# Performance work log

Measured on AMD Instinct MI355X. Metric: run time of the kernel, lower is better.

## Reference

```python
import jax, jax.numpy as jnp
import numpy as np

B, S, E, H, R = 2, 2048, 1024, 16, 8
D = E // H  # head depth = 64


def setup_inputs() -> dict:
    key = jax.random.key(0)
    ks = jax.random.split(key, 16)
    sd = 1.0 / np.sqrt(E)
    inp = {
        'q': jax.random.normal(ks[0], (B, S, E), jnp.float32),
        'k': jax.random.normal(ks[1], (B, S, E), jnp.float32),
        'v': jax.random.normal(ks[2], (B, S, E), jnp.float32),
        # Q projection (Dense + LoRA)
        'wq': jax.random.normal(ks[3], (E, E), jnp.float32) * sd,
        'bq': jnp.zeros((E,), jnp.float32),
        'wq_a': jax.random.normal(ks[4], (E, R), jnp.float32) * sd,
        'wq_b': jax.random.normal(ks[5], (R, E), jnp.float32) * 0.01,
        # K projection (plain Dense)
        'wk': jax.random.normal(ks[6], (E, E), jnp.float32) * sd,
        'bk': jnp.zeros((E,), jnp.float32),
        # V projection (Dense + LoRA)
        'wv': jax.random.normal(ks[7], (E, E), jnp.float32) * sd,
        'bv': jnp.zeros((E,), jnp.float32),
        'wv_a': jax.random.normal(ks[8], (E, R), jnp.float32) * sd,
        'wv_b': jax.random.normal(ks[9], (R, E), jnp.float32) * 0.01,
        # output projection
        'wo': jax.random.normal(ks[10], (E, E), jnp.float32) * sd,
        'bo': jnp.zeros((E,), jnp.float32),
    }
    return inp


def _lora_dense(x, w, b, w_a, w_b):
    # Dense(x) + (x @ A) @ B
    return x @ w + b + (x @ w_a) @ w_b


def _split_heads(x):
    # [B,S,E] -> [B,H,S,D]
    return x.reshape(B, S, H, D).transpose(0, 2, 1, 3)


def reference(q, k, v, wq, bq, wq_a, wq_b, wk, bk, wv, bv, wv_a, wv_b, wo, bo):
    qh = _split_heads(_lora_dense(q, wq, bq, wq_a, wq_b))
    kh = _split_heads(k @ wk + bk)
    vh = _split_heads(_lora_dense(v, wv, bv, wv_a, wv_b))
    # scaled dot-product attention per head
    scale = 1.0 / jnp.sqrt(jnp.asarray(D, jnp.float32))
    logits = jnp.einsum('bhqd,bhkd->bhqk', qh, kh) * scale
    attn = jax.nn.softmax(logits, axis=-1)
    out = jnp.einsum('bhqk,bhkd->bhqd', attn, vh)  # [B,H,S,D]
    out = out.transpose(0, 2, 1, 3).reshape(B, S, E)
    return out @ wo + bo
```

## Files before the change

kernel.cpp:

```cpp
#include <hip/hip_runtime.h>

typedef __attribute__((ext_vector_type(8))) _Float16 f16x8;
typedef __attribute__((ext_vector_type(4))) _Float16 f16x4;
typedef __attribute__((ext_vector_type(4))) float f32x4;

static __device__ __forceinline__ f16x4 pack4(float a, float b, float c, float d) {
    f16x4 r;
    auto p0 = __builtin_amdgcn_cvt_pkrtz(a, b);
    auto p1 = __builtin_amdgcn_cvt_pkrtz(c, d);
    r[0] = p0[0]; r[1] = p0[1]; r[2] = p1[0]; r[3] = p1[1];
    return r;
}

static __device__ __forceinline__ f16x8 cvt8(float4 u0, float4 u1) {
    f16x8 r;
    auto p = __builtin_amdgcn_cvt_pkrtz(u0.x, u0.y); r[0] = p[0]; r[1] = p[1];
    p = __builtin_amdgcn_cvt_pkrtz(u0.z, u0.w);      r[2] = p[0]; r[3] = p[1];
    p = __builtin_amdgcn_cvt_pkrtz(u1.x, u1.y);      r[4] = p[0]; r[5] = p[1];
    p = __builtin_amdgcn_cvt_pkrtz(u1.z, u1.w);      r[6] = p[0]; r[7] = p[1];
    return r;
}

static __device__ __forceinline__ void gll16(const void* g, void* l) {
    __builtin_amdgcn_global_load_lds(
        (const __attribute__((address_space(1))) unsigned int*)g,
        (__attribute__((address_space(3))) unsigned int*)l, 16, 0, 0);
}

__global__ __launch_bounds__(256) void prep16(const float* __restrict__ q, const float* __restrict__ k,
                                              const float* __restrict__ v, _Float16* __restrict__ o) {
    const float* X = blockIdx.y == 0 ? q : blockIdx.y == 1 ? k : v;
    _Float16* O = o + (size_t)blockIdx.y * 4194304;
    const int i = (blockIdx.x * 256 + threadIdx.x) * 8;
    *(f16x8*)&O[i] = cvt8(*(const float4*)&X[i], *(const float4*)&X[i + 4]);
}

__global__ __launch_bounds__(256) void tsplit_w16(const float* __restrict__ w0, const float* __restrict__ w1,
                                                  const float* __restrict__ w2, const float* __restrict__ w3,
                                                  _Float16* __restrict__ th) {
    const float* W = blockIdx.z == 0 ? w0 : blockIdx.z == 1 ? w1 : blockIdx.z == 2 ? w2 : w3;
    _Float16* oh = th + (size_t)blockIdx.z * 1048576;
    __shared__ float t[64][65];
    const int tid = threadIdx.x;
    const int kt = blockIdx.x, nb = blockIdx.y;
    const int k0 = kt * 64, n0 = nb * 64;
    const int c = tid & 15, r = tid >> 4;
#pragma unroll
    for (int i = 0; i < 4; ++i) {
        const int row = r + i * 16;
        const float4 v4 = *(const float4*)&W[(size_t)(k0 + row) * 1024 + n0 + c * 4];
        t[c * 4 + 0][row] = v4.x;
        t[c * 4 + 1][row] = v4.y;
        t[c * 4 + 2][row] = v4.z;
        t[c * 4 + 3][row] = v4.w;
    }
    __syncthreads();
    const size_t tb = (size_t)(nb * 16 + kt) * 4096;
#pragma unroll
    for (int i = 0; i < 2; ++i) {
        const int cid = tid * 2 + i;
        const int rr = cid >> 3, cc = cid & 7;
        const int ksrc = (cc ^ (rr & 7)) * 8;
        f16x8 hv;
#pragma unroll
        for (int j = 0; j < 8; ++j) hv[j] = (_Float16)t[rr][ksrc + j];
        *(f16x8*)&oh[tb + cid * 8] = hv;
    }
}

__global__ __launch_bounds__(256) void lora_xa2(const float* __restrict__ X0, const float* __restrict__ WA0,
                                                float* __restrict__ XA0,
                                                const float* __restrict__ X1, const float* __restrict__ WA1,
                                                float* __restrict__ XA1) {
    const float* X = blockIdx.y == 0 ? X0 : X1;
    const float* WA = blockIdx.y == 0 ? WA0 : WA1;
    float* XA = blockIdx.y == 0 ? XA0 : XA1;
    const int tid = threadIdx.x;
    const int w = tid >> 6, lane = tid & 63;
    const int m = blockIdx.x * 4 + w;
    const float* xrow = X + (size_t)m * 1024;
    float s[8] = {};
#pragma unroll
    for (int i = 0; i < 4; ++i) {
        const int k = lane * 4 + i * 256;
        const float4 x4 = *(const float4*)&xrow[k];
        const float xs[4] = {x4.x, x4.y, x4.z, x4.w};
#pragma unroll
        for (int j = 0; j < 4; ++j) {
            const float* wr = WA + (size_t)(k + j) * 8;
            const float xv = xs[j];
#pragma unroll
            for (int rr = 0; rr < 8; ++rr) s[rr] = fmaf(xv, wr[rr], s[rr]);
        }
    }
#pragma unroll
    for (int rr = 0; rr < 8; ++rr) {
        float v = s[rr];
        v += __shfl_xor(v, 32);
        v += __shfl_xor(v, 16);
        v += __shfl_xor(v, 8);
        v += __shfl_xor(v, 4);
        v += __shfl_xor(v, 2);
        v += __shfl_xor(v, 1);
        if (lane == 0) XA[(size_t)m * 8 + rr] = v;
    }
}

template <int OUT, bool LORA>
__global__ __launch_bounds__(256) void gemm_v3(const _Float16* __restrict__ A,
                                               const _Float16* __restrict__ Bt,
                                               const float* __restrict__ bias,
                                               const float* __restrict__ XA,
                                               const float* __restrict__ WB,
                                               float scale,
                                               void* __restrict__ outp) {
    __shared__ _Float16 Ahs[2][4096], Bhs[2][4096];
    const int tid = threadIdx.x;
    const int w = tid >> 6, l = tid & 63;
    const int lm = l & 15, g = l >> 4;
    const int wm = w >> 1, wn = w & 1;
    const int m0 = blockIdx.x * 64, nb = blockIdx.y, n0 = nb * 64;

    const int lr = l >> 3;
    const int ksw = ((l & 7) ^ lr) * 8;
    const _Float16* Asrc0 = A + (size_t)(m0 + w * 16 + lr) * 1024 + ksw;
    const _Float16* Asrc1 = A + (size_t)(m0 + w * 16 + 8 + lr) * 1024 + ksw;
    const _Float16* Bsrc0 = Bt + (size_t)nb * 65536 + (w * 128 + l) * 8;
    const _Float16* Bsrc1 = Bt + (size_t)nb * 65536 + (w * 128 + 64 + l) * 8;
    const int adst0 = w * 1024, adst1 = w * 1024 + 512;

    int afo[2][2], bfo[2][2];
#pragma unroll
    for (int t = 0; t < 2; ++t)
#pragma unroll
        for (int kc = 0; kc < 2; ++kc) {
            const int ar = wm * 32 + t * 16 + lm;
            const int br = wn * 32 + t * 16 + lm;
            afo[t][kc] = ar * 64 + (((kc * 4 + g) ^ (ar & 7)) * 8);
            bfo[t][kc] = br * 64 + (((kc * 4 + g) ^ (br & 7)) * 8);
        }

    f32x4 acc[2][2] = {};

#define STAGE(buf, kt)                                  \
    {                                                   \
        const int ko = (kt) * 64;                       \
        const int bo = (kt) * 4096;                     \
        gll16(Asrc0 + ko, &Ahs[buf][adst0]);            \
        gll16(Asrc1 + ko, &Ahs[buf][adst1]);            \
        gll16(Bsrc0 + bo, &Bhs[buf][adst0]);            \
        gll16(Bsrc1 + bo, &Bhs[buf][adst1]);            \
    }

    STAGE(0, 0)
    __syncthreads();

    for (int kt = 0; kt < 16; ++kt) {
        const int cur = kt & 1;
        if (kt < 15) STAGE(cur ^ 1, kt + 1)
        const _Float16* Ac = &Ahs[cur][0];
        const _Float16* Bc = &Bhs[cur][0];
#pragma unroll
        for (int kc = 0; kc < 2; ++kc) {
            f16x8 ah[2], bh[2];
#pragma unroll
            for (int i = 0; i < 2; ++i) {
                ah[i] = *(const f16x8*)&Ac[afo[i][kc]];
                bh[i] = *(const f16x8*)&Bc[bfo[i][kc]];
            }
            __builtin_amdgcn_s_setprio(1);
#pragma unroll
            for (int mt = 0; mt < 2; ++mt)
#pragma unroll
                for (int nt = 0; nt < 2; ++nt)
                    acc[mt][nt] = __builtin_amdgcn_mfma_f32_16x16x32_f16(ah[mt], bh[nt], acc[mt][nt], 0, 0, 0);
            __builtin_amdgcn_s_setprio(0);
        }
        __syncthreads();
    }
#undef STAGE

    const int nbase = n0 + wn * 32;
    const int head = nb;
    float bias2[2];
#pragma unroll
    for (int nt = 0; nt < 2; ++nt) bias2[nt] = bias[nbase + nt * 16 + lm];
    float wbv[8][2];
    if (LORA) {
#pragma unroll
        for (int rr = 0; rr < 8; ++rr)
#pragma unroll
            for (int nt = 0; nt < 2; ++nt) wbv[rr][nt] = WB[rr * 1024 + nbase + nt * 16 + lm];
    }
#pragma unroll
    for (int mt = 0; mt < 2; ++mt) {
        float ov[2][4];
#pragma unroll
        for (int r = 0; r < 4; ++r) {
            const int m = m0 + wm * 32 + mt * 16 + g * 4 + r;
            float xa8[8];
            if (LORA) {
#pragma unroll
                for (int rr = 0; rr < 8; ++rr) xa8[rr] = XA[(size_t)m * 8 + rr];
            }
#pragma unroll
            for (int nt = 0; nt < 2; ++nt) {
                float o = acc[mt][nt][r] + bias2[nt];
                if (LORA) {
#pragma unroll
                    for (int rr = 0; rr < 8; ++rr) o = fmaf(xa8[rr], wbv[rr][nt], o);
                }
                o *= scale;
                ov[nt][r] = o;
                if (OUT == 0) {
                    ((float*)outp)[(size_t)m * 1024 + nbase + nt * 16 + lm] = o;
                } else if (OUT == 1) {
                    const int b = m >> 11, s = m & 2047;
                    ((_Float16*)outp)[((size_t)(b * 16 + head) * 2048 + s) * 64 + wn * 32 + nt * 16 + lm] = (_Float16)o;
                }
            }
        }
        if (OUT == 2) {
            const int b = m0 >> 11;
            const int sb = (m0 & 2047) + wm * 32 + mt * 16 + g * 4;
#pragma unroll
            for (int nt = 0; nt < 2; ++nt) {
                const int d = wn * 32 + nt * 16 + lm;
                const f16x4 pv = pack4(ov[nt][0], ov[nt][1], ov[nt][2], ov[nt][3]);
                *(f16x4*)&((_Float16*)outp)[((size_t)(b * 16 + head) * 64 + d) * 2048 + sb] = pv;
            }
        }
    }
}

__global__ __launch_bounds__(256, 2) void flash_attn9(const _Float16* __restrict__ qh,
                                                      const _Float16* __restrict__ kh,
                                                      const _Float16* __restrict__ vT,
                                                      _Float16* __restrict__ ao) {
    __shared__ _Float16 Ks[2][4096];
    __shared__ _Float16 Vs[2][4096];
    const int tid = threadIdx.x;
    const int w = tid >> 6, l = tid & 63;
    const int m = l & 15, g = l >> 4;
    const int bh = blockIdx.x & 31, qt = blockIdx.x >> 5;
    const _Float16* Qb = qh + (size_t)bh * 131072;
    const _Float16* Kb = kh + (size_t)bh * 131072;
    const _Float16* Vb = vT + (size_t)bh * 131072;
    const int q0 = qt * 128 + w * 32;

    f16x8 qf[2][2];
#pragma unroll
    for (int qg = 0; qg < 2; ++qg) {
        const _Float16* qrow = Qb + (size_t)(q0 + qg * 16 + m) * 64 + g * 8;
        qf[qg][0] = *(const f16x8*)(qrow);
        qf[qg][1] = *(const f16x8*)(qrow + 32);
    }

    const int r0 = tid >> 3, c0 = tid & 7;
    const int r1 = (tid + 256) >> 3;
    const int kgl0 = r0 * 64 + c0 * 8;
    const int kgl1 = r1 * 64 + c0 * 8;
    const int kso0 = r0 * 64 + ((c0 ^ (r0 & 7)) * 8);
    const int kso1 = r1 * 64 + ((c0 ^ (r1 & 7)) * 8);
    const size_t vgl0 = (size_t)r0 * 2048 + c0 * 8;
    const size_t vgl1 = (size_t)r1 * 2048 + c0 * 8;

    int koff[4][2];
#pragma unroll
    for (int nt = 0; nt < 4; ++nt)
#pragma unroll
        for (int kc = 0; kc < 2; ++kc) {
            const int kv = nt * 16 + m;
            koff[nt][kc] = kv * 64 + (((kc * 4 + g) ^ (kv & 7)) * 8);
        }
    int voff[4][4];
#pragma unroll
    for (int dt = 0; dt < 4; ++dt)
#pragma unroll
        for (int nt = 0; nt < 4; ++nt) {
            const int d = dt * 16 + m;
            voff[dt][nt] = d * 64 + (((nt * 2 + (g >> 1)) ^ (d & 7)) * 8) + (g & 1) * 4;
        }

    f32x4 acc_o[2][4] = {};
    f32x4 acc_l[2] = {};
    const f16x4 onesf = {(_Float16)1.f, (_Float16)1.f, (_Float16)1.f, (_Float16)1.f};

    {
        const f16x8 ka = *(const f16x8*)(Kb + kgl0);
        const f16x8 kb2 = *(const f16x8*)(Kb + kgl1);
        const f16x8 va = *(const f16x8*)(Vb + vgl0);
        const f16x8 vb2 = *(const f16x8*)(Vb + vgl1);
        *(f16x8*)(&Ks[0][0] + kso0) = ka;
        *(f16x8*)(&Ks[0][0] + kso1) = kb2;
        *(f16x8*)(&Vs[0][0] + kso0) = va;
        *(f16x8*)(&Vs[0][0] + kso1) = vb2;
    }
    __syncthreads();

    for (int t = 0; t < 32; ++t) {
        const int cur = t & 1;
        f16x8 ka, kb2, va, vb2;
        if (t < 31) {
            const int koI = (t + 1) * 4096;
            const int voI = (t + 1) * 64;
            ka = *(const f16x8*)(Kb + koI + kgl0);
            kb2 = *(const f16x8*)(Kb + koI + kgl1);
            va = *(const f16x8*)(Vb + voI + vgl0);
            vb2 = *(const f16x8*)(Vb + voI + vgl1);
        }

        const _Float16* Kc = &Ks[cur][0];
        const _Float16* Vc = &Vs[cur][0];

        f32x4 s[2][4] = {};
        __builtin_amdgcn_s_setprio(1);
#pragma unroll
        for (int nt = 0; nt < 4; ++nt)
#pragma unroll
            for (int kc = 0; kc < 2; ++kc) {
                const f16x8 kf = *(const f16x8*)(Kc + koff[nt][kc]);
                s[0][nt] = __builtin_amdgcn_mfma_f32_16x16x32_f16(kf, qf[0][kc], s[0][nt], 0, 0, 0);
                s[1][nt] = __builtin_amdgcn_mfma_f32_16x16x32_f16(kf, qf[1][kc], s[1][nt], 0, 0, 0);
            }
        __builtin_amdgcn_s_setprio(0);

        f16x4 pf[2][4];
#pragma unroll
        for (int qg = 0; qg < 2; ++qg)
#pragma unroll
            for (int nt = 0; nt < 4; ++nt)
                pf[qg][nt] = pack4(exp2f(s[qg][nt][0]), exp2f(s[qg][nt][1]),
                                   exp2f(s[qg][nt][2]), exp2f(s[qg][nt][3]));

        __builtin_amdgcn_s_setprio(1);
#pragma unroll
        for (int nt = 0; nt < 4; ++nt) {
            acc_l[0] = __builtin_amdgcn_mfma_f32_16x16x16f16(onesf, pf[0][nt], acc_l[0], 0, 0, 0);
            acc_l[1] = __builtin_amdgcn_mfma_f32_16x16x16f16(onesf, pf[1][nt], acc_l[1], 0, 0, 0);
#pragma unroll
            for (int dt = 0; dt < 4; ++dt) {
                const f16x4 vf = *(const f16x4*)(Vc + voff[dt][nt]);
                acc_o[0][dt] = __builtin_amdgcn_mfma_f32_16x16x16f16(vf, pf[0][nt], acc_o[0][dt], 0, 0, 0);
                acc_o[1][dt] = __builtin_amdgcn_mfma_f32_16x16x16f16(vf, pf[1][nt], acc_o[1][dt], 0, 0, 0);
            }
        }
        __builtin_amdgcn_s_setprio(0);

        if (t < 31) {
            const int nxt = cur ^ 1;
            *(f16x8*)(&Ks[nxt][0] + kso0) = ka;
            *(f16x8*)(&Ks[nxt][0] + kso1) = kb2;
            *(f16x8*)(&Vs[nxt][0] + kso0) = va;
            *(f16x8*)(&Vs[nxt][0] + kso1) = vb2;
        }
        __syncthreads();
    }

    const int b = bh >> 4, h = bh & 15;
#pragma unroll
    for (int qg = 0; qg < 2; ++qg) {
        const float inv = 1.f / acc_l[qg][0];
        const int srow = q0 + qg * 16 + m;
        _Float16* orow = ao + ((size_t)(b * 2048 + srow)) * 1024 + h * 64;
#pragma unroll
        for (int dt = 0; dt < 4; ++dt) {
            const f16x4 o = pack4(acc_o[qg][dt][0] * inv, acc_o[qg][dt][1] * inv,
                                  acc_o[qg][dt][2] * inv, acc_o[qg][dt][3] * inv);
            *(f16x4*)&orow[dt * 16 + g * 4] = o;
        }
    }
}

extern "C" void kernel_launch(void* const* d_in, const int* in_sizes, int n_in,
                              void* d_out, int out_size, void* d_ws, size_t ws_size,
                              hipStream_t stream) {
    const float* q    = (const float*)d_in[0];
    const float* k    = (const float*)d_in[1];
    const float* v    = (const float*)d_in[2];
    const float* wq   = (const float*)d_in[3];
    const float* bq   = (const float*)d_in[4];
    const float* wq_a = (const float*)d_in[5];
    const float* wq_b = (const float*)d_in[6];
    const float* wk   = (const float*)d_in[7];
    const float* bk   = (const float*)d_in[8];
    const float* wv   = (const float*)d_in[9];
    const float* bv   = (const float*)d_in[10];
    const float* wv_a = (const float*)d_in[11];
    const float* wv_b = (const float*)d_in[12];
    const float* wo   = (const float*)d_in[13];
    const float* bo   = (const float*)d_in[14];
    float* out = (float*)d_out;

    char* wsb = (char*)d_ws;
    _Float16* Wt   = (_Float16*)(wsb);
    _Float16* a16  = (_Float16*)(wsb + (8u << 20));
    _Float16* aoF  = a16;
    _Float16* qhF  = (_Float16*)(wsb + (32u << 20));
    _Float16* khF  = (_Float16*)(wsb + (40u << 20));
    _Float16* vTF  = (_Float16*)(wsb + (48u << 20));
    float* xaq     = (float*)(wsb + (56u << 20));
    float* xav     = (float*)(wsb + (56u << 20) + (128u << 10));

    const dim3 ggrid(64, 16);
    const float qscale = 0.18033688f;

    tsplit_w16<<<dim3(16, 16, 4), 256, 0, stream>>>(wq, wk, wv, wo, Wt);
    lora_xa2<<<dim3(1024, 2), 256, 0, stream>>>(q, wq_a, xaq, v, wv_a, xav);
    prep16<<<dim3(2048, 3), 256, 0, stream>>>(q, k, v, a16);

    gemm_v3<1, true><<<ggrid, 256, 0, stream>>>(a16, Wt, bq, xaq, wq_b, qscale, qhF);
    gemm_v3<1, false><<<ggrid, 256, 0, stream>>>(a16 + 4194304, Wt + 1048576, bk, nullptr, nullptr, 1.f, khF);
    gemm_v3<2, true><<<ggrid, 256, 0, stream>>>(a16 + 8388608, Wt + 2097152, bv, xav, wv_b, 1.f, vTF);

    flash_attn9<<<512, 256, 0, stream>>>(qhF, khF, vTF, aoF);

    gemm_v3<0, false><<<ggrid, 256, 0, stream>>>(aoF, Wt + 3145728, bo, nullptr, nullptr, 1.f, out);
}
```

Measured before the change: 170.4 us.

## Use 128x64 GEMM tiles with 32x32x16 MFMA instructions

The projection GEMMs now compute a 128x64 output tile per block instead of 64x64, halving the grid and reusing each staged B tile across twice as many rows. The inner loop switches from 16x16x32 MFMAs to 32x32x16 MFMAs, each wave producing a 64x32 sub-tile, and the epilogue index mapping is rewritten for the new accumulator layout. This cuts B-operand global and LDS traffic per output and issues fewer, larger MFMAs. In exchange it uses more LDS and registers per block and launches 512 blocks instead of 1024, which may lower occupancy and load balance across CUs.

```diff
diff --git a/kernel.cpp b/kernel.cpp
--- a/kernel.cpp
+++ b/kernel.cpp
@@ -3,6 +3,7 @@
 typedef __attribute__((ext_vector_type(8))) _Float16 f16x8;
 typedef __attribute__((ext_vector_type(4))) _Float16 f16x4;
 typedef __attribute__((ext_vector_type(4))) float f32x4;
+typedef __attribute__((ext_vector_type(16))) float f32x16;
 
 static __device__ __forceinline__ f16x4 pack4(float a, float b, float c, float d) {
     f16x4 r;
@@ -107,49 +108,57 @@
 }
 
 template <int OUT, bool LORA>
-__global__ __launch_bounds__(256) void gemm_v3(const _Float16* __restrict__ A,
+__global__ __launch_bounds__(256) void gemm_v5(const _Float16* __restrict__ A,
                                                const _Float16* __restrict__ Bt,
                                                const float* __restrict__ bias,
                                                const float* __restrict__ XA,
                                                const float* __restrict__ WB,
                                                float scale,
                                                void* __restrict__ outp) {
-    __shared__ _Float16 Ahs[2][4096], Bhs[2][4096];
+    __shared__ _Float16 Ahs[2][8192];
+    __shared__ _Float16 Bhs[2][4096];
     const int tid = threadIdx.x;
     const int w = tid >> 6, l = tid & 63;
-    const int lm = l & 15, g = l >> 4;
+    const int ln = l & 31, hi = l >> 5;
     const int wm = w >> 1, wn = w & 1;
-    const int m0 = blockIdx.x * 64, nb = blockIdx.y, n0 = nb * 64;
+    const int m0 = blockIdx.x * 128, nb = blockIdx.y;
 
     const int lr = l >> 3;
     const int ksw = ((l & 7) ^ lr) * 8;
-    const _Float16* Asrc0 = A + (size_t)(m0 + w * 16 + lr) * 1024 + ksw;
-    const _Float16* Asrc1 = A + (size_t)(m0 + w * 16 + 8 + lr) * 1024 + ksw;
+    const _Float16* Asrc[4];
+    int adst[4];
+#pragma unroll
+    for (int j = 0; j < 4; ++j) {
+        Asrc[j] = A + (size_t)(m0 + w * 32 + j * 8 + lr) * 1024 + ksw;
+        adst[j] = w * 2048 + j * 512;
+    }
     const _Float16* Bsrc0 = Bt + (size_t)nb * 65536 + (w * 128 + l) * 8;
     const _Float16* Bsrc1 = Bt + (size_t)nb * 65536 + (w * 128 + 64 + l) * 8;
-    const int adst0 = w * 1024, adst1 = w * 1024 + 512;
-
-    int afo[2][2], bfo[2][2];
-#pragma unroll
-    for (int t = 0; t < 2; ++t)
-#pragma unroll
-        for (int kc = 0; kc < 2; ++kc) {
-            const int ar = wm * 32 + t * 16 + lm;
-            const int br = wn * 32 + t * 16 + lm;
-            afo[t][kc] = ar * 64 + (((kc * 4 + g) ^ (ar & 7)) * 8);
-            bfo[t][kc] = br * 64 + (((kc * 4 + g) ^ (br & 7)) * 8);
-        }
-
-    f32x4 acc[2][2] = {};
-
-#define STAGE(buf, kt)                                  \
-    {                                                   \
-        const int ko = (kt) * 64;                       \
-        const int bo = (kt) * 4096;                     \
-        gll16(Asrc0 + ko, &Ahs[buf][adst0]);            \
-        gll16(Asrc1 + ko, &Ahs[buf][adst1]);            \
-        gll16(Bsrc0 + bo, &Bhs[buf][adst0]);            \
-        gll16(Bsrc1 + bo, &Bhs[buf][adst1]);            \
+    const int bdst0 = w * 1024, bdst1 = w * 1024 + 512;
+
+    int afo[2][4], bfo[4];
+#pragma unroll
+    for (int s = 0; s < 4; ++s) {
+        const int c = s * 2 + hi;
+#pragma unroll
+        for (int mt = 0; mt < 2; ++mt) {
+            const int ar = wm * 64 + mt * 32 + ln;
+            afo[mt][s] = ar * 64 + ((c ^ (ln & 7)) * 8);
+        }
+        const int br = wn * 32 + ln;
+        bfo[s] = br * 64 + ((c ^ (ln & 7)) * 8);
+    }
+
+    f32x16 acc[2] = {};
+
+#define STAGE(buf, kt)                                       \
+    {                                                        \
+        const int ko = (kt) * 64;                            \
+        const int bo = (kt) * 4096;                          \
+        _Pragma("unroll") for (int j = 0; j < 4; ++j)        \
+            gll16(Asrc[j] + ko, &Ahs[buf][adst[j]]);         \
+        gll16(Bsrc0 + bo, &Bhs[buf][bdst0]);                 \
+        gll16(Bsrc1 + bo, &Bhs[buf][bdst1]);                 \
     }
 
     STAGE(0, 0)
@@ -161,73 +170,64 @@
         const _Float16* Ac = &Ahs[cur][0];
         const _Float16* Bc = &Bhs[cur][0];
 #pragma unroll
-        for (int kc = 0; kc < 2; ++kc) {
-            f16x8 ah[2], bh[2];
-#pragma unroll
-            for (int i = 0; i < 2; ++i) {
-                ah[i] = *(const f16x8*)&Ac[afo[i][kc]];
-                bh[i] = *(const f16x8*)&Bc[bfo[i][kc]];
-            }
+        for (int s = 0; s < 4; ++s) {
+            const f16x8 a0 = *(const f16x8*)&Ac[afo[0][s]];
+            const f16x8 a1 = *(const f16x8*)&Ac[afo[1][s]];
+            const f16x8 bfrag = *(const f16x8*)&Bc[bfo[s]];
             __builtin_amdgcn_s_setprio(1);
-#pragma unroll
-            for (int mt = 0; mt < 2; ++mt)
-#pragma unroll
-                for (int nt = 0; nt < 2; ++nt)
-                    acc[mt][nt] = __builtin_amdgcn_mfma_f32_16x16x32_f16(ah[mt], bh[nt], acc[mt][nt], 0, 0, 0);
+            acc[0] = __builtin_amdgcn_mfma_f32_32x32x16_f16(a0, bfrag, acc[0], 0, 0, 0);
+            acc[1] = __builtin_amdgcn_mfma_f32_32x32x16_f16(a1, bfrag, acc[1], 0, 0, 0);
             __builtin_amdgcn_s_setprio(0);
         }
         __syncthreads();
     }
 #undef STAGE
 
-    const int nbase = n0 + wn * 32;
-    const int head = nb;
-    float bias2[2];
-#pragma unroll
-    for (int nt = 0; nt < 2; ++nt) bias2[nt] = bias[nbase + nt * 16 + lm];
-    float wbv[8][2];
+    const int nl = nb * 64 + wn * 32 + ln;
+    const float biasl = bias[nl];
+    float wbl[8];
     if (LORA) {
 #pragma unroll
-        for (int rr = 0; rr < 8; ++rr)
-#pragma unroll
-            for (int nt = 0; nt < 2; ++nt) wbv[rr][nt] = WB[rr * 1024 + nbase + nt * 16 + lm];
+        for (int rr = 0; rr < 8; ++rr) wbl[rr] = WB[rr * 1024 + nl];
     }
 #pragma unroll
     for (int mt = 0; mt < 2; ++mt) {
-        float ov[2][4];
-#pragma unroll
-        for (int r = 0; r < 4; ++r) {
-            const int m = m0 + wm * 32 + mt * 16 + g * 4 + r;
-            float xa8[8];
-            if (LORA) {
-#pragma unroll
-                for (int rr = 0; rr < 8; ++rr) xa8[rr] = XA[(size_t)m * 8 + rr];
-            }
-#pragma unroll
-            for (int nt = 0; nt < 2; ++nt) {
-                float o = acc[mt][nt][r] + bias2[nt];
+        const int bm = m0 + wm * 64 + mt * 32;
+#pragma unroll
+        for (int q2 = 0; q2 < 4; ++q2) {
+            float ov[4];
+#pragma unroll
+            for (int r4 = 0; r4 < 4; ++r4) {
+                const int reg = q2 * 4 + r4;
+                const int m = bm + r4 + 8 * q2 + 4 * hi;
+                float o = acc[mt][reg] + biasl;
                 if (LORA) {
-#pragma unroll
-                    for (int rr = 0; rr < 8; ++rr) o = fmaf(xa8[rr], wbv[rr][nt], o);
+                    const float4 xa0 = *(const float4*)&XA[(size_t)m * 8];
+                    const float4 xa1 = *(const float4*)&XA[(size_t)m * 8 + 4];
+                    o = fmaf(xa0.x, wbl[0], o);
+                    o = fmaf(xa0.y, wbl[1], o);
+                    o = fmaf(xa0.z, wbl[2], o);
+                    o = fmaf(xa0.w, wbl[3], o);
+                    o = fmaf(xa1.x, wbl[4], o);
+                    o = fmaf(xa1.y, wbl[5], o);
+                    o = fmaf(xa1.z, wbl[6], o);
+                    o = fmaf(xa1.w, wbl[7], o);
                 }
                 o *= scale;
-                ov[nt][r] = o;
+                ov[r4] = o;
                 if (OUT == 0) {
-                    ((float*)outp)[(size_t)m * 1024 + nbase + nt * 16 + lm] = o;
+                    ((float*)outp)[(size_t)m * 1024 + nl] = o;
                 } else if (OUT == 1) {
                     const int b = m >> 11, s = m & 2047;
-                    ((_Float16*)outp)[((size_t)(b * 16 + head) * 2048 + s) * 64 + wn * 32 + nt * 16 + lm] = (_Float16)o;
+                    ((_Float16*)outp)[((size_t)(b * 16 + nb) * 2048 + s) * 64 + wn * 32 + ln] = (_Float16)o;
                 }
             }
-        }
-        if (OUT == 2) {
-            const int b = m0 >> 11;
-            const int sb = (m0 & 2047) + wm * 32 + mt * 16 + g * 4;
-#pragma unroll
-            for (int nt = 0; nt < 2; ++nt) {
-                const int d = wn * 32 + nt * 16 + lm;
-                const f16x4 pv = pack4(ov[nt][0], ov[nt][1], ov[nt][2], ov[nt][3]);
-                *(f16x4*)&((_Float16*)outp)[((size_t)(b * 16 + head) * 64 + d) * 2048 + sb] = pv;
+            if (OUT == 2) {
+                const int b = bm >> 11;
+                const int s0 = (bm & 2047) + 8 * q2 + 4 * hi;
+                const int d = wn * 32 + ln;
+                *(f16x4*)&((_Float16*)outp)[((size_t)(b * 16 + nb) * 64 + d) * 2048 + s0] =
+                    pack4(ov[0], ov[1], ov[2], ov[3]);
             }
         }
     }
@@ -402,18 +402,18 @@
     float* xaq     = (float*)(wsb + (56u << 20));
     float* xav     = (float*)(wsb + (56u << 20) + (128u << 10));
 
-    const dim3 ggrid(64, 16);
+    const dim3 ggrid(32, 16);
     const float qscale = 0.18033688f;
 
     tsplit_w16<<<dim3(16, 16, 4), 256, 0, stream>>>(wq, wk, wv, wo, Wt);
     lora_xa2<<<dim3(1024, 2), 256, 0, stream>>>(q, wq_a, xaq, v, wv_a, xav);
     prep16<<<dim3(2048, 3), 256, 0, stream>>>(q, k, v, a16);
 
-    gemm_v3<1, true><<<ggrid, 256, 0, stream>>>(a16, Wt, bq, xaq, wq_b, qscale, qhF);
-    gemm_v3<1, false><<<ggrid, 256, 0, stream>>>(a16 + 4194304, Wt + 1048576, bk, nullptr, nullptr, 1.f, khF);
-    gemm_v3<2, true><<<ggrid, 256, 0, stream>>>(a16 + 8388608, Wt + 2097152, bv, xav, wv_b, 1.f, vTF);
+    gemm_v5<1, true><<<ggrid, 256, 0, stream>>>(a16, Wt, bq, xaq, wq_b, qscale, qhF);
+    gemm_v5<1, false><<<ggrid, 256, 0, stream>>>(a16 + 4194304, Wt + 1048576, bk, nullptr, nullptr, 1.f, khF);
+    gemm_v5<2, true><<<ggrid, 256, 0, stream>>>(a16 + 8388608, Wt + 2097152, bv, xav, wv_b, 1.f, vTF);
 
     flash_attn9<<<512, 256, 0, stream>>>(qhF, khF, vTF, aoF);
 
-    gemm_v3<0, false><<<ggrid, 256, 0, stream>>>(aoF, Wt + 3145728, bo, nullptr, nullptr, 1.f, out);
-}
+    gemm_v5<0, false><<<ggrid, 256, 0, stream>>>(aoF, Wt + 3145728, bo, nullptr, nullptr, 1.f, out);
+}
```

After: 182.1 us. 1.07x slower.
